# Performance work log

Hardware: AMD Instinct MI355X
Metric: run time of the kernel (lower is better)

The kernel has to match this reference:

```python
import jax, jax.numpy as jnp
import numpy as np

# Router hyperparameters (from init_kwargs)
E = 64        # num_routed_experts
K = 6         # moe_router_topk
G = 8         # num_expert_groups
TG = 3        # topk_group
ALPHA = 0.001 # aux_loss_alpha
EPG = E // G  # experts per group


def setup_inputs() -> dict:
    key = jax.random.key(0)
    k1, k2 = jax.random.split(key)
    hidden_states = jax.random.normal(k1, (4, 4096, 4096), dtype=jnp.float32)
    # kaiming_uniform-ish scale for the gate weight [E, H]
    bound = 1.0 / np.sqrt(4096)
    weight = jax.random.uniform(k2, (E, 4096), dtype=jnp.float32,
                                minval=-bound, maxval=bound)
    return {"hidden_states": hidden_states, "weight": weight}


def reference(hidden_states, weight):
    B, S, H = hidden_states.shape
    T = B * S
    x = hidden_states.reshape(T, H).astype(jnp.float32)
    # gate GEMM + softmax scoring
    logits = jnp.einsum('th,eh->te', x, weight.astype(jnp.float32))  # [T, E]
    scores = jax.nn.softmax(logits, axis=-1)
    # group-limited greedy: keep only experts in the top-TG groups (by group max)
    group_scores = scores.reshape(T, G, EPG).max(axis=-1)            # [T, G]
    _, group_idx = jax.lax.top_k(group_scores, TG)                   # [T, TG]
    group_mask = jnp.zeros((T, G), scores.dtype).at[
        jnp.arange(T)[:, None], group_idx].set(1.0)                  # [T, G]
    score_mask = jnp.repeat(group_mask, EPG, axis=-1)                # [T, E]
    tmp_scores = jnp.where(score_mask > 0, scores, 0.0)
    topk_weight, topk_idx = jax.lax.top_k(tmp_scores, K)             # [T, K]
    # norm_topk_prob = True and top_k > 1 -> normalize
    topk_weight = topk_weight / (topk_weight.sum(axis=-1, keepdims=True) + 1e-20)
    # sequence-level aux loss (seq_aux=True, training, alpha > 0)
    idx_aux = topk_idx.reshape(B, S * K)                             # [B, S*K]
    ce = jax.vmap(lambda idx: jnp.zeros(E, jnp.float32).at[idx].add(1.0))(idx_aux)
    ce = ce / (S * K / E)                                            # [B, E]
    aux_loss = (ce * scores.reshape(B, S, E).mean(axis=1)).sum(axis=1).mean() * ALPHA
    return topk_idx, topk_weight, aux_loss
```

## Files before the change

### kernel.cpp

```cpp
#include <hip/hip_runtime.h>
#include <math.h>

#define TTOK   16384
#define HDIM   4096
#define ENUM   64
#define KTOP   6
#define GNUM   8
#define TGK    3
#define BBATCH 4
#define SSEQ   4096
#define ALPHAC 0.001f

#define KSPLIT 4
#define KSL    (HDIM / KSPLIT)
#define TM     256
#define TE     32
#define BK     32
#define NIT    (KSL / BK)

#define AS3(p) ((__attribute__((address_space(3))) void*)(p))
#define AS1(p) ((const __attribute__((address_space(1))) void*)(p))

typedef float wvec16 __attribute__((ext_vector_type(16)));

__global__ __launch_bounds__(256)
void pack_w(const float* __restrict__ W, float* __restrict__ Wp) {
    const int gid = blockIdx.x * 256 + threadIdx.x;
    const int k4 = gid >> 6, e = gid & 63;
    float4 v = *(const float4*)(W + (size_t)e * HDIM + k4 * 4);
    *(float4*)(Wp + (size_t)gid * 4) = v;
}

__global__ __launch_bounds__(512, 4)
void gate_gemm(const float* __restrict__ X, const float* __restrict__ Wp,
               float* __restrict__ lp) {
    __shared__ __align__(16) float Xs[2][TM * BK];

    const int tid = threadIdx.x;
    const int w   = __builtin_amdgcn_readfirstlane(tid >> 6);
    const int l   = tid & 63;
    const int lm7 = l & 7;

    const int id     = blockIdx.x;
    const int linear = (id & 7) * 64 + (id >> 3);
    const int eh     = linear & 1;
    const int ts     = linear >> 1;
    const int tile   = ts & 63;
    const int slice  = ts >> 6;
    const int T0     = tile * TM;
    const int k0     = slice * KSL;
    const int E0     = eh * TE + w * 4;

    const int trow = l >> 3;
    const int kswz = ((l & 7) ^ trow) << 2;
    const float* gs = X + (size_t)(T0 + w * 8 + trow) * HDIM + k0 + kswz;

#define STAGE(buf_, it_) do {                                                   \
    const size_t go_ = (size_t)(it_) * BK;                                      \
    _Pragma("unroll")                                                           \
    for (int r_ = 0; r_ < 4; ++r_)                                              \
        __builtin_amdgcn_global_load_lds(                                       \
            AS1(gs + (size_t)r_ * 64 * HDIM + go_),                             \
            AS3(&Xs[buf_][r_ * 2048 + w * 256]), 16, 0, 0);                     \
} while (0)

    float acc[4][4];
#pragma unroll
    for (int g = 0; g < 4; ++g)
#pragma unroll
        for (int j = 0; j < 4; ++j) acc[g][j] = 0.f;

    const int k4base = k0 >> 2;

    STAGE(0, 0);

    for (int it = 0; it < NIT; ++it) {
        __syncthreads();
        if (it + 1 < NIT) STAGE((it + 1) & 1, it + 1);

        const float* xb = Xs[it & 1];
        const int k4it  = k4base + it * (BK / 4);
#pragma unroll
        for (int kq = 0; kq < 8; ++kq) {
            const wvec16 wv = *(const wvec16*)(Wp + ((size_t)(k4it + kq) * ENUM + E0) * 4);
            const int slot = (kq ^ lm7) << 2;
#pragma unroll
            for (int g = 0; g < 4; ++g) {
                const float4 xv = *(const float4*)(xb + (g * 64 + l) * BK + slot);
#pragma unroll
                for (int j = 0; j < 4; ++j) {
                    acc[g][j] = fmaf(xv.x, wv[4 * j + 0], acc[g][j]);
                    acc[g][j] = fmaf(xv.y, wv[4 * j + 1], acc[g][j]);
                    acc[g][j] = fmaf(xv.z, wv[4 * j + 2], acc[g][j]);
                    acc[g][j] = fmaf(xv.w, wv[4 * j + 3], acc[g][j]);
                }
            }
        }
    }

    float* dst = lp + (size_t)slice * TTOK * ENUM + (size_t)(T0 + l) * ENUM + E0;
#pragma unroll
    for (int g = 0; g < 4; ++g)
        *(float4*)(dst + (size_t)g * 64 * ENUM) =
            make_float4(acc[g][0], acc[g][1], acc[g][2], acc[g][3]);
#undef STAGE
}

#define RTOK 64
__global__ __launch_bounds__(256)
void router_topk(const float* __restrict__ lp,
                 float* __restrict__ out_idx, float* __restrict__ out_w,
                 float* __restrict__ ssum_g, int* __restrict__ cnt_g) {
    __shared__ float Ls[RTOK * 67];
    __shared__ float s_m[RTOK], s_inv[RTOK];
    __shared__ float s_ssum[ENUM];
    __shared__ int   s_cnt[ENUM];

    const int tid = threadIdx.x;
    const int t0  = blockIdx.x * RTOK;
    if (tid < ENUM) { s_cnt[tid] = 0; s_ssum[tid] = 0.f; }

#pragma unroll
    for (int r = 0; r < 4; ++r) {
        const int q  = r * 256 + tid;
        const int t  = q >> 4, c4 = q & 15;
        const size_t base = (size_t)(t0 + t) * ENUM + c4 * 4;
        float4 v = *(const float4*)(lp + base);
#pragma unroll
        for (int h = 1; h < KSPLIT; ++h) {
            float4 u = *(const float4*)(lp + (size_t)h * TTOK * ENUM + base);
            v.x += u.x; v.y += u.y; v.z += u.z; v.w += u.w;
        }
        float* d = Ls + t * 67 + c4 * 4;
        d[0] = v.x; d[1] = v.y; d[2] = v.z; d[3] = v.w;
    }
    __syncthreads();

    if (tid < RTOK) {
        const float* row = Ls + tid * 67;

        float gm[GNUM];
#pragma unroll
        for (int g = 0; g < GNUM; ++g) {
            float mg = row[g * 8];
#pragma unroll
            for (int j = 1; j < 8; ++j) mg = fmaxf(mg, row[g * 8 + j]);
            gm[g] = mg;
        }
        float m = gm[0];
#pragma unroll
        for (int g = 1; g < GNUM; ++g) m = fmaxf(m, gm[g]);

        int selmask = 0;
#pragma unroll
        for (int g = 0; g < GNUM; ++g) {
            int rank = 0;
#pragma unroll
            for (int g2 = 0; g2 < GNUM; ++g2)
                rank += (gm[g2] > gm[g]) || (gm[g2] == gm[g] && g2 < g);
            selmask |= (rank < TGK) << g;
        }

        float v0=-1.f,v1=-1.f,v2=-1.f,v3=-1.f,v4=-1.f,v5=-1.f;
        float i0=0.f,i1=0.f,i2=0.f,i3=0.f,i4=0.f,i5=0.f;
        float s = 0.f;
#pragma unroll
        for (int e = 0; e < ENUM; ++e) {
            const float ex = __expf(row[e] - m);
            s += ex;
            const float cand = ((selmask >> (e >> 3)) & 1) ? ex : -1.0f;
            const float fe = (float)e;
            const bool b0 = cand > v0, b1 = cand > v1, b2 = cand > v2,
                       b3 = cand > v3, b4 = cand > v4, b5 = cand > v5;
            v5 = b4 ? v4 : (b5 ? cand : v5);  i5 = b4 ? i4 : (b5 ? fe : i5);
            v4 = b3 ? v3 : (b4 ? cand : v4);  i4 = b3 ? i3 : (b4 ? fe : i4);
            v3 = b2 ? v2 : (b3 ? cand : v3);  i3 = b2 ? i2 : (b3 ? fe : i3);
            v2 = b1 ? v1 : (b2 ? cand : v2);  i2 = b1 ? i1 : (b2 ? fe : i2);
            v1 = b0 ? v0 : (b1 ? cand : v1);  i1 = b0 ? i0 : (b1 ? fe : i1);
            v0 = b0 ? cand : v0;              i0 = b0 ? fe : i0;
        }
        const float invw = 1.0f / (v0 + v1 + v2 + v3 + v4 + v5);
        const int t = t0 + tid;
        float* oi = out_idx + (size_t)t * KTOP;
        float* ow = out_w   + (size_t)t * KTOP;
        oi[0]=i0; oi[1]=i1; oi[2]=i2; oi[3]=i3; oi[4]=i4; oi[5]=i5;
        ow[0]=v0*invw; ow[1]=v1*invw; ow[2]=v2*invw;
        ow[3]=v3*invw; ow[4]=v4*invw; ow[5]=v5*invw;

        atomicAdd(&s_cnt[(int)i0], 1); atomicAdd(&s_cnt[(int)i1], 1);
        atomicAdd(&s_cnt[(int)i2], 1); atomicAdd(&s_cnt[(int)i3], 1);
        atomicAdd(&s_cnt[(int)i4], 1); atomicAdd(&s_cnt[(int)i5], 1);
        s_m[tid] = m; s_inv[tid] = 1.0f / s;
    }
    __syncthreads();

    {
        const int e = tid & 63, strip = tid >> 6;
        float acc = 0.f;
#pragma unroll
        for (int i = 0; i < RTOK / 4; ++i) {
            const int t = strip * (RTOK / 4) + i;
            acc += __expf(Ls[t * 67 + e] - s_m[t]) * s_inv[t];
        }
        atomicAdd(&s_ssum[e], acc);
    }
    __syncthreads();

    const int b = t0 / SSEQ;
    if (tid < ENUM) {
        atomicAdd(&ssum_g[b * ENUM + tid], s_ssum[tid]);
        atomicAdd(&cnt_g[b * ENUM + tid], s_cnt[tid]);
    }
}

__global__ __launch_bounds__(256)
void aux_loss(const float* __restrict__ ssum_g, const int* __restrict__ cnt_g,
              float* __restrict__ out_aux) {
    const int tid = threadIdx.x;
    float v = (float)cnt_g[tid] * (float)ENUM / ((float)SSEQ * (float)KTOP)
            * (ssum_g[tid] / (float)SSEQ);
#pragma unroll
    for (int off = 32; off; off >>= 1) v += __shfl_xor(v, off);
    __shared__ float red[4];
    if ((tid & 63) == 0) red[tid >> 6] = v;
    __syncthreads();
    if (tid == 0)
        out_aux[0] = (red[0] + red[1] + red[2] + red[3]) * (ALPHAC / (float)BBATCH);
}

extern "C" void kernel_launch(void* const* d_in, const int* in_sizes, int n_in,
                              void* d_out, int out_size, void* d_ws, size_t ws_size,
                              hipStream_t stream) {
    const float* X = (const float*)d_in[0];
    const float* W = (const float*)d_in[1];

    float* out     = (float*)d_out;
    float* out_idx = out;
    float* out_w   = out + (size_t)TTOK * KTOP;
    float* out_aux = out + (size_t)2 * TTOK * KTOP;

    float* lp     = (float*)d_ws;
    float* Wp     = lp + (size_t)KSPLIT * TTOK * ENUM;
    float* ssum_g = Wp + (size_t)HDIM * ENUM;
    int*   cnt_g  = (int*)(ssum_g + BBATCH * ENUM);

    hipMemsetAsync(ssum_g, 0, BBATCH * ENUM * (sizeof(float) + sizeof(int)), stream);

    pack_w<<<(HDIM / 4) * ENUM / 256, 256, 0, stream>>>(W, Wp);
    gate_gemm<<<512, 512, 0, stream>>>(X, Wp, lp);
    router_topk<<<TTOK / RTOK, 256, 0, stream>>>(lp, out_idx, out_w, ssum_g, cnt_g);
    aux_loss<<<1, 256, 0, stream>>>(ssum_g, cnt_g, out_aux);
}
```

Measured before the change: 424.0 us.

## Cover all 64 experts per block and double the K-split

Each gate GEMM block now computes all 64 experts, 8 per wave, instead of half of them. This means every X tile is read from global memory once rather than twice. The K dimension is split 8 ways instead of 4 so the grid keeps the same block count, and the L2-friendly block swizzle is dropped. The trade-offs are doubled accumulator registers, which may reduce occupancy under launch_bounds(512,4), and twice as many partial logits for the router to reduce. Unless the router kernel (not shown) was also updated, KSPLIT=8 is consistent only if its reduction loop uses the macro.

```diff
diff --git a/kernel.cpp b/kernel.cpp
--- a/kernel.cpp
+++ b/kernel.cpp
@@ -11,10 +11,9 @@
 #define SSEQ   4096
 #define ALPHAC 0.001f
 
-#define KSPLIT 4
+#define KSPLIT 8
 #define KSL    (HDIM / KSPLIT)
 #define TM     256
-#define TE     32
 #define BK     32
 #define NIT    (KSL / BK)
 
@@ -41,15 +40,12 @@
     const int l   = tid & 63;
     const int lm7 = l & 7;
 
-    const int id     = blockIdx.x;
-    const int linear = (id & 7) * 64 + (id >> 3);
-    const int eh     = linear & 1;
-    const int ts     = linear >> 1;
-    const int tile   = ts & 63;
-    const int slice  = ts >> 6;
-    const int T0     = tile * TM;
-    const int k0     = slice * KSL;
-    const int E0     = eh * TE + w * 4;
+    const int id    = blockIdx.x;
+    const int tile  = id >> 3;
+    const int slice = id & 7;
+    const int T0    = tile * TM;
+    const int k0    = slice * KSL;
+    const int E0    = w * 8;
 
     const int trow = l >> 3;
     const int kswz = ((l & 7) ^ trow) << 2;
@@ -64,11 +60,11 @@
             AS3(&Xs[buf_][r_ * 2048 + w * 256]), 16, 0, 0);                     \
 } while (0)
 
-    float acc[4][4];
+    float acc[4][8];
 #pragma unroll
     for (int g = 0; g < 4; ++g)
 #pragma unroll
-        for (int j = 0; j < 4; ++j) acc[g][j] = 0.f;
+        for (int j = 0; j < 8; ++j) acc[g][j] = 0.f;
 
     const int k4base = k0 >> 2;
 
@@ -82,17 +78,26 @@
         const int k4it  = k4base + it * (BK / 4);
 #pragma unroll
         for (int kq = 0; kq < 8; ++kq) {
-            const wvec16 wv = *(const wvec16*)(Wp + ((size_t)(k4it + kq) * ENUM + E0) * 4);
+            const float* wp = Wp + ((size_t)(k4it + kq) * ENUM + E0) * 4;
+            const wvec16 wa = *(const wvec16*)(wp);
+            const wvec16 wb = *(const wvec16*)(wp + 16);
             const int slot = (kq ^ lm7) << 2;
 #pragma unroll
             for (int g = 0; g < 4; ++g) {
                 const float4 xv = *(const float4*)(xb + (g * 64 + l) * BK + slot);
 #pragma unroll
                 for (int j = 0; j < 4; ++j) {
-                    acc[g][j] = fmaf(xv.x, wv[4 * j + 0], acc[g][j]);
-                    acc[g][j] = fmaf(xv.y, wv[4 * j + 1], acc[g][j]);
-                    acc[g][j] = fmaf(xv.z, wv[4 * j + 2], acc[g][j]);
-                    acc[g][j] = fmaf(xv.w, wv[4 * j + 3], acc[g][j]);
+                    acc[g][j] = fmaf(xv.x, wa[4 * j + 0], acc[g][j]);
+                    acc[g][j] = fmaf(xv.y, wa[4 * j + 1], acc[g][j]);
+                    acc[g][j] = fmaf(xv.z, wa[4 * j + 2], acc[g][j]);
+                    acc[g][j] = fmaf(xv.w, wa[4 * j + 3], acc[g][j]);
+                }
+#pragma unroll
+                for (int j = 0; j < 4; ++j) {
+                    acc[g][4 + j] = fmaf(xv.x, wb[4 * j + 0], acc[g][4 + j]);
+                    acc[g][4 + j] = fmaf(xv.y, wb[4 * j + 1], acc[g][4 + j]);
+                    acc[g][4 + j] = fmaf(xv.z, wb[4 * j + 2], acc[g][4 + j]);
+                    acc[g][4 + j] = fmaf(xv.w, wb[4 * j + 3], acc[g][4 + j]);
                 }
             }
         }
@@ -100,9 +105,11 @@
 
     float* dst = lp + (size_t)slice * TTOK * ENUM + (size_t)(T0 + l) * ENUM + E0;
 #pragma unroll
-    for (int g = 0; g < 4; ++g)
-        *(float4*)(dst + (size_t)g * 64 * ENUM) =
-            make_float4(acc[g][0], acc[g][1], acc[g][2], acc[g][3]);
+    for (int g = 0; g < 4; ++g) {
+        float* d = dst + (size_t)g * 64 * ENUM;
+        *(float4*)(d + 0) = make_float4(acc[g][0], acc[g][1], acc[g][2], acc[g][3]);
+        *(float4*)(d + 4) = make_float4(acc[g][4], acc[g][5], acc[g][6], acc[g][7]);
+    }
 #undef STAGE
 }
 
```

After: 416.7 us. About the same (-1.7%).
